# Kernel tuning notes

Measured on AMD Instinct MI355X. Metric: run time of the kernel, lower is better.

The kernel has to match this reference:

```python
import jax, jax.numpy as jnp
import numpy as np
from jax import lax

KERNEL_SIZE = 3
DILATION = 1
STRIDE = 1


def setup_inputs() -> dict:
    key = jax.random.key(0)
    k1, k2, k3, k4 = jax.random.split(key, 4)
    B, C_in, L = 8, 256, 4096
    C_out = 256
    out_len = L - DILATION * (KERNEL_SIZE - 1)  # 4094, 'valid' conv
    x = jax.random.normal(k1, (B, C_in, L), dtype=jnp.float32)
    offsets = jax.random.normal(k2, (B, 1, out_len, KERNEL_SIZE), dtype=jnp.float32)
    fan_in = C_in * KERNEL_SIZE
    weight = jax.random.normal(k3, (C_out, C_in, KERNEL_SIZE), dtype=jnp.float32) / np.sqrt(fan_in)
    bias = jax.random.normal(k4, (C_out,), dtype=jnp.float32) / np.sqrt(fan_in)
    return {"x": x, "offsets": offsets, "weight": weight, "bias": bias}


def reference(x, offsets, weight, bias):
    # x: [B, C, L]; offsets: [B, 1, out_len, K]; weight: [C_out, C, K]
    B, C, L = x.shape
    out_len = offsets.shape[-2]
    K = weight.shape[-1]
    dtype = x.dtype

    # dilated kernel sample positions: linspace(0, dilation*(K-1), K)
    dil_pos = (jnp.arange(K, dtype=dtype) * DILATION)  # [K]
    t0s = (jnp.arange(out_len, dtype=dtype) * STRIDE)[:, None]  # [out_len, 1]

    # continuous sample locations, constrained to [t0, t0 + max(dil_pos)]
    T = t0s + dil_pos + offsets  # [B, 1, out_len, K]
    T = jnp.clip(T, t0s, t0s + dil_pos[-1])

    # integer neighbors (indices are non-differentiable)
    U0 = lax.stop_gradient(
        jnp.clip(jnp.floor(T), 0, L - 2).astype(jnp.int32)
    )  # [B, 1, out_len, K]
    U1 = U0 + 1

    def gather(idx):
        # idx: [B, 1, out_len, K] -> gather along L, broadcast over channels
        flat = jnp.broadcast_to(idx.reshape(B, 1, out_len * K), (B, C, out_len * K))
        return jnp.take_along_axis(x, flat, axis=2).reshape(B, C, out_len, K)

    x0 = gather(U0)
    x1 = gather(U1)

    # linear-interpolation weights (tent kernel), broadcast [B,1,out_len,K]
    w0 = jnp.maximum(0.0, 1.0 - jnp.abs(U0.astype(dtype) - T))
    w1 = jnp.maximum(0.0, 1.0 - jnp.abs(U1.astype(dtype) - T))

    interp = w0 * x0 + w1 * x1  # [B, C, out_len, K]

    # conv1d(flatten(interp), weight, stride=K) == per-position K-tap contraction
    out = jnp.einsum("bctk,ock->bot", interp, weight) + bias[None, :, None]
    return out  # [B, C_out, out_len]
```

## Files before the change

kernel.cpp:

```cpp
#include <hip/hip_runtime.h>
#include <stdint.h>


constexpr int CIN  = 256;
constexpr int LX   = 4096;
constexpr int KT   = 3;
constexpr int OUTL = 4094;
constexpr int COUT = 256;
constexpr int WPOS = 68;
constexpr int NQ   = 24;
constexpr int EPIW = 68;
constexpr int NIT  = 2176;

typedef __attribute__((ext_vector_type(8))) short bf16x8;
typedef __attribute__((ext_vector_type(4))) float f32x4;
typedef __attribute__((ext_vector_type(16))) float f32x16;

__device__ __forceinline__ short f2bf(float f) {
  union { float f; uint32_t u; } v; v.f = f;
  return (short)((v.u + 0x8000u) >> 16);
}
__device__ __forceinline__ float bf2f(short s) {
  union { uint32_t u; float f; } v;
  v.u = ((uint32_t)(uint16_t)s) << 16;
  return v.f;
}
__device__ __forceinline__ float4 loadx4(const float* p, int l) {
  if (l + 3 < LX) return *(const float4*)(p + l);
  float4 v; v.x = v.y = v.z = v.w = 0.f;
  if (l + 0 < LX) v.x = p[l + 0];
  if (l + 1 < LX) v.y = p[l + 1];
  if (l + 2 < LX) v.z = p[l + 2];
  return v;
}

__global__ __launch_bounds__(256) void pack_weights_kernel(
    const float* __restrict__ w, short* __restrict__ ap) {
  const int gid = blockIdx.x * 256 + threadIdx.x;
  if (gid >= NQ * 2 * 8 * 64) return;
  const int l   = gid & 63;
  const int mf  = (gid >> 6) & 7;
  const int h   = (gid >> 9) & 1;
  const int q   = gid >> 10;
  const int ch  = q / 12;
  const int ks  = q % 12;
  const int tap = ks >> 2;
  const int c0  = ch * 128 + (ks & 3) * 32 + h * 16 + (l >> 5) * 8;
  const int row = mf * 32 + (l & 31);
  bf16x8 v;
  #pragma unroll
  for (int j = 0; j < 8; ++j) {
    v[j] = f2bf(w[((size_t)row * CIN + c0 + j) * KT + tap]);
  }
  *(bf16x8*)(ap + (size_t)gid * 8) = v;
}

__global__ __launch_bounds__(512, 4) void deform_gemm_kernel(
    const float* __restrict__ x, const float* __restrict__ off,
    const short* __restrict__ ap, const float* __restrict__ bias,
    float* __restrict__ out) {

  __shared__ __align__(16) char smem[2 * 17408 + 16384 + 1024];
  short* Xt0   = (short*)smem;
  short* Xt1   = (short*)(smem + 17408);
  short* Bp    = (short*)(smem + 34816);
  float* Epi   = (float*)smem;
  float* biasS = (float*)(smem + 51200);

  const int tid  = threadIdx.x;
  const int lane = tid & 63;
  const int wid  = tid >> 6;
  const int l31  = lane & 31;
  const int lh   = lane >> 5;

  const int b    = blockIdx.x & 7;
  const int rest = blockIdx.x >> 3;
  const int th   = rest & 1;
  const int tt   = rest >> 1;
  const int t0   = tt * 128 + th * 64;

  int xc[5], xg[5];
  #pragma unroll
  for (int r = 0; r < 5; ++r) {
    const int idx = r * 512 + tid;
    xc[r] = idx / 17;
    xg[r] = idx - xc[r] * 17;
  }

  float w0m[3], w1m[3];
  int   d0m[3];
  {
    const int t = t0 + (tid & 63);
    #pragma unroll
    for (int k = 0; k < KT; ++k) {
      float w0 = 0.f, w1 = 0.f; int d0 = 0;
      if (t < OUTL) {
        const float o = off[((size_t)b * OUTL + t) * KT + k];
        float T = (float)(t + k) + o;
        T = fminf(fmaxf(T, (float)t), (float)(t + 2));
        int U0 = (int)T;
        if (U0 > LX - 2) U0 = LX - 2;
        w1 = T - (float)U0;
        w0 = 1.f - w1;
        d0 = U0 - t0;
      }
      w0m[k] = w0; w1m[k] = w1; d0m[k] = d0;
    }
  }
  if (tid < COUT) biasS[tid] = bias[tid];

  f32x16 acc0 = {0.f,0.f,0.f,0.f,0.f,0.f,0.f,0.f,0.f,0.f,0.f,0.f,0.f,0.f,0.f,0.f};
  f32x16 acc1 = {0.f,0.f,0.f,0.f,0.f,0.f,0.f,0.f,0.f,0.f,0.f,0.f,0.f,0.f,0.f,0.f};

  const float* xb = x + (size_t)b * CIN * LX;

  const short* apw = ap + wid * 512 + lane * 8;
  bf16x8 aC0 = *(const bf16x8*)apw;
  bf16x8 aC1 = *(const bf16x8*)(apw + 4096);

  float4 xv[5];
  #pragma unroll
  for (int r = 0; r < 5; ++r)
    if (r * 512 + tid < NIT) xv[r] = loadx4(xb + (size_t)xc[r] * LX, t0 + 4 * xg[r]);
  #pragma unroll
  for (int r = 0; r < 5; ++r)
    if (r * 512 + tid < NIT) {
      const float fe[4] = {xv[r].x, xv[r].y, xv[r].z, xv[r].w};
      #pragma unroll
      for (int e = 0; e < 4; ++e) {
        const int pos = xg[r] * 4 + e;
        Xt0[(pos * 128 + xc[r]) ^ ((pos & 7) << 3)] = f2bf(fe[e]);
      }
    }
  __syncthreads();

  #pragma unroll
  for (int r = 0; r < 5; ++r)
    if (r * 512 + tid < NIT)
      xv[r] = loadx4(xb + (size_t)(128 + xc[r]) * LX, t0 + 4 * xg[r]);

  #pragma unroll 1
  for (int ch = 0; ch < 2; ++ch) {
    short* Xc = ch ? Xt1 : Xt0;

    #pragma unroll
    for (int tap = 0; tap < KT; ++tap) {
      if (tap | ch) __syncthreads();
      {
        const int tq = tid & 63;
        const int c0 = (tid >> 6) * 16;
        const float w0 = w0m[tap], w1 = w1m[tap];
        const int   d0 = d0m[tap];
        const int sw0 = (d0 & 7) << 3;
        const int sw1 = ((d0 + 1) & 7) << 3;
        const int r0i = d0 * 128, r1i = (d0 + 1) * 128;
        const bf16x8 r0a = *(const bf16x8*)&Xc[(r0i + c0)     ^ sw0];
        const bf16x8 r0b = *(const bf16x8*)&Xc[(r0i + c0 + 8) ^ sw0];
        const bf16x8 r1a = *(const bf16x8*)&Xc[(r1i + c0)     ^ sw1];
        const bf16x8 r1b = *(const bf16x8*)&Xc[(r1i + c0 + 8) ^ sw1];
        bf16x8 o1, o2;
        #pragma unroll
        for (int j = 0; j < 8; ++j) {
          o1[j] = f2bf(bf2f(r0a[j]) * w0 + bf2f(r1a[j]) * w1);
          o2[j] = f2bf(bf2f(r0b[j]) * w0 + bf2f(r1b[j]) * w1);
        }
        const int swt = (tq & 7) << 3;
        *(bf16x8*)&Bp[(tq * 128 + c0)     ^ swt] = o1;
        *(bf16x8*)&Bp[(tq * 128 + c0 + 8) ^ swt] = o2;
      }
      __syncthreads();

      #pragma unroll 1
      for (int csub = 0; csub < 4; ++csub) {
        const int q  = ch * 12 + tap * 4 + csub;
        const int qn = q < NQ - 1 ? q + 1 : NQ - 1;
        const bf16x8 aN0 = *(const bf16x8*)(apw + (size_t)qn * 8192);
        const bf16x8 aN1 = *(const bf16x8*)(apw + (size_t)qn * 8192 + 4096);

        const int cbase = csub * 32 + lh * 8;
        const int ta = l31,      swa = (ta & 7) << 3;
        const int tb = 32 + l31, swb = (tb & 7) << 3;
        const bf16x8 b00 = *(const bf16x8*)&Bp[(ta * 128 + cbase)      ^ swa];
        const bf16x8 b01 = *(const bf16x8*)&Bp[(ta * 128 + cbase + 16) ^ swa];
        const bf16x8 b10 = *(const bf16x8*)&Bp[(tb * 128 + cbase)      ^ swb];
        const bf16x8 b11 = *(const bf16x8*)&Bp[(tb * 128 + cbase + 16) ^ swb];

        acc0 = __builtin_amdgcn_mfma_f32_32x32x16_bf16(aC0, b00, acc0, 0, 0, 0);
        acc0 = __builtin_amdgcn_mfma_f32_32x32x16_bf16(aC1, b01, acc0, 0, 0, 0);
        acc1 = __builtin_amdgcn_mfma_f32_32x32x16_bf16(aC0, b10, acc1, 0, 0, 0);
        acc1 = __builtin_amdgcn_mfma_f32_32x32x16_bf16(aC1, b11, acc1, 0, 0, 0);

        aC0 = aN0; aC1 = aN1;
      }
    }

    if (ch == 0) {
      #pragma unroll
      for (int r = 0; r < 5; ++r)
        if (r * 512 + tid < NIT) {
          const float fe[4] = {xv[r].x, xv[r].y, xv[r].z, xv[r].w};
          #pragma unroll
          for (int e = 0; e < 4; ++e) {
            const int pos = xg[r] * 4 + e;
            Xt1[(pos * 128 + xc[r]) ^ ((pos & 7) << 3)] = f2bf(fe[e]);
          }
        }
    }
  }

  const size_t obase = (size_t)b * COUT * OUTL;
  #pragma unroll
  for (int p = 0; p < 4; ++p) {
    __syncthreads();
    if ((wid >> 1) == p) {
      const int lrb = (wid & 1) * 32;
      #pragma unroll
      for (int r = 0; r < 16; ++r) {
        const int rowl = (r & 3) + 8 * (r >> 2) + 4 * lh;
        const int grow = p * 64 + lrb + rowl;
        Epi[(lrb + rowl) * EPIW + l31]      = acc0[r] + biasS[grow];
        Epi[(lrb + rowl) * EPIW + 32 + l31] = acc1[r] + biasS[grow];
      }
    }
    __syncthreads();
    const int rr = tid >> 3;
    const int c8 = (tid & 7) * 8;
    float* op = out + obase + (size_t)(p * 64 + rr) * OUTL + t0 + c8;
    const f32x4 v0 = *(const f32x4*)&Epi[rr * EPIW + c8];
    const f32x4 v1 = *(const f32x4*)&Epi[rr * EPIW + c8 + 4];
    if (t0 + c8 + 7 < OUTL) {
      *(f32x4*)op = v0;
      *(f32x4*)(op + 4) = v1;
    } else {
      #pragma unroll
      for (int e = 0; e < 4; ++e) {
        if (t0 + c8 + e < OUTL)     op[e]     = v0[e];
        if (t0 + c8 + 4 + e < OUTL) op[4 + e] = v1[e];
      }
    }
  }
}

extern "C" void kernel_launch(void* const* d_in, const int* in_sizes, int n_in,
                              void* d_out, int out_size, void* d_ws, size_t ws_size,
                              hipStream_t stream) {
  const float* x    = (const float*)d_in[0];
  const float* off  = (const float*)d_in[1];
  const float* wgt  = (const float*)d_in[2];
  const float* bias = (const float*)d_in[3];
  float* out  = (float*)d_out;
  short* ap   = (short*)d_ws;

  pack_weights_kernel<<<dim3(NQ * 2 * 8 * 64 / 256), dim3(256), 0, stream>>>(wgt, ap);
  deform_gemm_kernel<<<dim3(512), dim3(512), 0, stream>>>(x, off, ap, bias, out);
}
```

Before: 44.10 us.

## Stagger second-half x prefetch and staging across taps to cut register pressure

Result: slower. 49.16 us (+11.5%).

```diff
diff --git a/kernel.cpp b/kernel.cpp
--- a/kernel.cpp
+++ b/kernel.cpp
@@ -7,7 +7,6 @@
 constexpr int KT   = 3;
 constexpr int OUTL = 4094;
 constexpr int COUT = 256;
-constexpr int WPOS = 68;
 constexpr int NQ   = 24;
 constexpr int EPIW = 68;
 constexpr int NIT  = 2176;
@@ -78,14 +77,6 @@
   const int th   = rest & 1;
   const int tt   = rest >> 1;
   const int t0   = tt * 128 + th * 64;
-
-  int xc[5], xg[5];
-  #pragma unroll
-  for (int r = 0; r < 5; ++r) {
-    const int idx = r * 512 + tid;
-    xc[r] = idx / 17;
-    xg[r] = idx - xc[r] * 17;
-  }
 
   float w0m[3], w1m[3];
   int   d0m[3];
@@ -119,25 +110,29 @@
   bf16x8 aC1 = *(const bf16x8*)(apw + 4096);
 
   float4 xv[5];
-  #pragma unroll
-  for (int r = 0; r < 5; ++r)
-    if (r * 512 + tid < NIT) xv[r] = loadx4(xb + (size_t)xc[r] * LX, t0 + 4 * xg[r]);
-  #pragma unroll
-  for (int r = 0; r < 5; ++r)
-    if (r * 512 + tid < NIT) {
+
+  #pragma unroll
+  for (int r = 0; r < 5; ++r) {
+    const int idx = r * 512 + tid;
+    if (idx < NIT) {
+      const int c = idx / 17, g = idx - c * 17;
+      xv[r] = loadx4(xb + (size_t)c * LX, t0 + 4 * g);
+    }
+  }
+  #pragma unroll
+  for (int r = 0; r < 5; ++r) {
+    const int idx = r * 512 + tid;
+    if (idx < NIT) {
+      const int c = idx / 17, g = idx - c * 17;
       const float fe[4] = {xv[r].x, xv[r].y, xv[r].z, xv[r].w};
       #pragma unroll
       for (int e = 0; e < 4; ++e) {
-        const int pos = xg[r] * 4 + e;
-        Xt0[(pos * 128 + xc[r]) ^ ((pos & 7) << 3)] = f2bf(fe[e]);
-      }
-    }
+        const int pos = g * 4 + e;
+        Xt0[(pos * 128 + c) ^ ((pos & 7) << 3)] = f2bf(fe[e]);
+      }
+    }
+  }
   __syncthreads();
-
-  #pragma unroll
-  for (int r = 0; r < 5; ++r)
-    if (r * 512 + tid < NIT)
-      xv[r] = loadx4(xb + (size_t)(128 + xc[r]) * LX, t0 + 4 * xg[r]);
 
   #pragma unroll 1
   for (int ch = 0; ch < 2; ++ch) {
@@ -146,6 +141,26 @@
     #pragma unroll
     for (int tap = 0; tap < KT; ++tap) {
       if (tap | ch) __syncthreads();
+      if (ch == 0 && tap > 0) {
+        const int rlo = (tap == 1) ? 0 : 3;
+        const int rhi = (tap == 1) ? 3 : 5;
+        #pragma unroll
+        for (int r = 0; r < 5; ++r) {
+          if (r >= rlo && r < rhi) {
+            const int idx = r * 512 + tid;
+            if (idx < NIT) {
+              const int c = idx / 17, g = idx - c * 17;
+              const float fe[4] = {xv[r].x, xv[r].y, xv[r].z, xv[r].w};
+              #pragma unroll
+              for (int e = 0; e < 4; ++e) {
+                const int pos = g * 4 + e;
+                Xt1[(pos * 128 + c) ^ ((pos & 7) << 3)] = f2bf(fe[e]);
+              }
+            }
+          }
+        }
+      }
+
       {
         const int tq = tid & 63;
         const int c0 = (tid >> 6) * 16;
@@ -154,21 +169,42 @@
         const int sw0 = (d0 & 7) << 3;
         const int sw1 = ((d0 + 1) & 7) << 3;
         const int r0i = d0 * 128, r1i = (d0 + 1) * 128;
-        const bf16x8 r0a = *(const bf16x8*)&Xc[(r0i + c0)     ^ sw0];
-        const bf16x8 r0b = *(const bf16x8*)&Xc[(r0i + c0 + 8) ^ sw0];
-        const bf16x8 r1a = *(const bf16x8*)&Xc[(r1i + c0)     ^ sw1];
-        const bf16x8 r1b = *(const bf16x8*)&Xc[(r1i + c0 + 8) ^ sw1];
-        bf16x8 o1, o2;
+        const int swt = (tq & 7) << 3;
+        {
+          const bf16x8 r0a = *(const bf16x8*)&Xc[(r0i + c0) ^ sw0];
+          const bf16x8 r1a = *(const bf16x8*)&Xc[(r1i + c0) ^ sw1];
+          bf16x8 o1;
+          #pragma unroll
+          for (int j = 0; j < 8; ++j)
+            o1[j] = f2bf(bf2f(r0a[j]) * w0 + bf2f(r1a[j]) * w1);
+          *(bf16x8*)&Bp[(tq * 128 + c0) ^ swt] = o1;
+        }
+        {
+          const bf16x8 r0b = *(const bf16x8*)&Xc[(r0i + c0 + 8) ^ sw0];
+          const bf16x8 r1b = *(const bf16x8*)&Xc[(r1i + c0 + 8) ^ sw1];
+          bf16x8 o2;
+          #pragma unroll
+          for (int j = 0; j < 8; ++j)
+            o2[j] = f2bf(bf2f(r0b[j]) * w0 + bf2f(r1b[j]) * w1);
+          *(bf16x8*)&Bp[(tq * 128 + c0 + 8) ^ swt] = o2;
+        }
+      }
+      __syncthreads();
+
+      if (ch == 0 && tap < 2) {
+        const int rlo = (tap == 0) ? 0 : 3;
+        const int rhi = (tap == 0) ? 3 : 5;
         #pragma unroll
-        for (int j = 0; j < 8; ++j) {
-          o1[j] = f2bf(bf2f(r0a[j]) * w0 + bf2f(r1a[j]) * w1);
-          o2[j] = f2bf(bf2f(r0b[j]) * w0 + bf2f(r1b[j]) * w1);
-        }
-        const int swt = (tq & 7) << 3;
-        *(bf16x8*)&Bp[(tq * 128 + c0)     ^ swt] = o1;
-        *(bf16x8*)&Bp[(tq * 128 + c0 + 8) ^ swt] = o2;
-      }
-      __syncthreads();
+        for (int r = 0; r < 5; ++r) {
+          if (r >= rlo && r < rhi) {
+            const int idx = r * 512 + tid;
+            if (idx < NIT) {
+              const int c = idx / 17, g = idx - c * 17;
+              xv[r] = loadx4(xb + (size_t)(128 + c) * LX, t0 + 4 * g);
+            }
+          }
+        }
+      }
 
       #pragma unroll 1
       for (int csub = 0; csub < 4; ++csub) {
@@ -180,31 +216,20 @@
         const int cbase = csub * 32 + lh * 8;
         const int ta = l31,      swa = (ta & 7) << 3;
         const int tb = 32 + l31, swb = (tb & 7) << 3;
-        const bf16x8 b00 = *(const bf16x8*)&Bp[(ta * 128 + cbase)      ^ swa];
-        const bf16x8 b01 = *(const bf16x8*)&Bp[(ta * 128 + cbase + 16) ^ swa];
-        const bf16x8 b10 = *(const bf16x8*)&Bp[(tb * 128 + cbase)      ^ swb];
-        const bf16x8 b11 = *(const bf16x8*)&Bp[(tb * 128 + cbase + 16) ^ swb];
-
-        acc0 = __builtin_amdgcn_mfma_f32_32x32x16_bf16(aC0, b00, acc0, 0, 0, 0);
-        acc0 = __builtin_amdgcn_mfma_f32_32x32x16_bf16(aC1, b01, acc0, 0, 0, 0);
-        acc1 = __builtin_amdgcn_mfma_f32_32x32x16_bf16(aC0, b10, acc1, 0, 0, 0);
-        acc1 = __builtin_amdgcn_mfma_f32_32x32x16_bf16(aC1, b11, acc1, 0, 0, 0);
-
+        {
+          const bf16x8 b00 = *(const bf16x8*)&Bp[(ta * 128 + cbase) ^ swa];
+          const bf16x8 b10 = *(const bf16x8*)&Bp[(tb * 128 + cbase) ^ swb];
+          acc0 = __builtin_amdgcn_mfma_f32_32x32x16_bf16(aC0, b00, acc0, 0, 0, 0);
+          acc1 = __builtin_amdgcn_mfma_f32_32x32x16_bf16(aC0, b10, acc1, 0, 0, 0);
+        }
+        {
+          const bf16x8 b01 = *(const bf16x8*)&Bp[(ta * 128 + cbase + 16) ^ swa];
+          const bf16x8 b11 = *(const bf16x8*)&Bp[(tb * 128 + cbase + 16) ^ swb];
+          acc0 = __builtin_amdgcn_mfma_f32_32x32x16_bf16(aC1, b01, acc0, 0, 0, 0);
+          acc1 = __builtin_amdgcn_mfma_f32_32x32x16_bf16(aC1, b11, acc1, 0, 0, 0);
+        }
         aC0 = aN0; aC1 = aN1;
       }
-    }
-
-    if (ch == 0) {
-      #pragma unroll
-      for (int r = 0; r < 5; ++r)
-        if (r * 512 + tid < NIT) {
-          const float fe[4] = {xv[r].x, xv[r].y, xv[r].z, xv[r].w};
-          #pragma unroll
-          for (int e = 0; e < 4; ++e) {
-            const int pos = xg[r] * 4 + e;
-            Xt1[(pos * 128 + xc[r]) ^ ((pos & 7) << 3)] = f2bf(fe[e]);
-          }
-        }
     }
   }
 
```
